# Performance work log

Hardware: AMD Instinct MI355X
Metric: run time of the kernel (lower is better)

The kernel has to match this reference:

```python
import jax, jax.numpy as jnp
import numpy as np


def setup_inputs() -> dict:
    key = jax.random.key(0)
    k1, k2, k3 = jax.random.split(key, 3)
    B, C, H, W = 4, 256, 96, 128
    F = 9
    return {
        "input1": jax.random.normal(k1, (B, C, H, W), dtype=jnp.float32),
        "input2": jax.random.normal(k2, (B, C, H, W), dtype=jnp.float32),
        "weights": jax.random.normal(k3, (C, F, F), dtype=jnp.float32),
        "filter_size": 9,
        "dilation": 2,
        "num_groups": 4,
    }


def _weighted_corr(input1, input2, weights, filter_size, dilation, num_groups):
    B, C, H, W = input1.shape
    F = filter_size
    G = num_groups
    Cg = C // G
    r = F // 2
    pad = r * dilation
    # zero-pad input2 spatially so out-of-bounds displacements contribute 0
    p2 = jnp.pad(input2, ((0, 0), (0, 0), (pad, pad), (pad, pad)))
    in1g = input1.reshape(B, G, Cg, H, W)
    outs = []  # one [B, G, H, W] map per window offset (dy, dx)
    for dy in range(F):
        for dx in range(F):
            shifted = p2[:, :, dy * dilation:dy * dilation + H,
                         dx * dilation:dx * dilation + W].reshape(B, G, Cg, H, W)
            wg = weights[:, dy, dx].reshape(G, Cg)
            outs.append(jnp.einsum('bgchw,bgchw,gc->bghw', in1g, shifted, wg))
    out = jnp.stack(outs, axis=2)  # [B, G, F*F, H, W]
    return out.reshape(B, G * F * F, H, W)


def reference(input1, input2, weights, filter_size, dilation, num_groups):
    return _weighted_corr(input1, input2, weights, filter_size, dilation, num_groups)
```

## Files before the change

kernel.cpp:

```cpp
#include <hip/hip_runtime.h>

#define B_   4
#define C_   256
#define H_   96
#define W_   128
#define F_   9
#define G_   4
#define CG   64
#define NC8  8
#define NO   81
#define HW_  (H_ * W_)

#define OROWS 4
#define TCOLS 144
#define PCOLS 72
#define NENT  (OROWS * 2 * PCOLS)
#define PNK   3

typedef _Float16 half2v __attribute__((ext_vector_type(2)));
typedef unsigned u32x4 __attribute__((ext_vector_type(4)));

__device__ __forceinline__ half2v u2h(unsigned u) {
    half2v h; __builtin_memcpy(&h, &u, 4); return h;
}
__device__ __forceinline__ unsigned h2u(half2v h) {
    unsigned u; __builtin_memcpy(&u, &h, 4); return u;
}
__device__ __forceinline__ half2v pkrtz(float a, float b) {
    auto r = __builtin_amdgcn_cvt_pkrtz(a, b);
    half2v h; __builtin_memcpy(&h, &r, 4); return h;
}
__device__ __forceinline__ unsigned pkrtz_u(float a, float b) {
    auto r = __builtin_amdgcn_cvt_pkrtz(a, b);
    unsigned u; __builtin_memcpy(&u, &r, 4); return u;
}

#if __has_builtin(__builtin_amdgcn_fdot2)
#define FDOT2(a, b, c) __builtin_amdgcn_fdot2((a), (b), (c), false)
#else
__device__ __forceinline__ float fdot2_fb(half2v a, half2v b, float c) {
    return c + (float)a[0] * (float)b[0] + (float)a[1] * (float)b[1];
}
#define FDOT2(a, b, c) fdot2_fb((a), (b), (c))
#endif

__device__ __forceinline__ int swz(int col2) {
    return col2 ^ ((col2 >> 3) & 7);
}

__global__ void pack_weights_kernel(const float* __restrict__ w,
                                    u32x4* __restrict__ wp) {
    int i = blockIdx.x * blockDim.x + threadIdx.x;
    if (i >= G_ * NC8 * NO) return;
    int o  = i % NO;
    int c8 = (i / NO) % NC8;
    int g  = i / (NO * NC8);
    const float* base = w + (size_t)(g * CG + 8 * c8) * NO + o;
    u32x4 r;
    r.x = pkrtz_u(base[0 * NO], base[1 * NO]);
    r.y = pkrtz_u(base[2 * NO], base[3 * NO]);
    r.z = pkrtz_u(base[4 * NO], base[5 * NO]);
    r.w = pkrtz_u(base[6 * NO], base[7 * NO]);
    wp[i] = r;
}

template <bool PACKED>
__global__ __launch_bounds__(256)
void wcorr_kernel(const float* __restrict__ in1, const float* __restrict__ in2,
                  const u32x4* __restrict__ wp, const float* __restrict__ wraw,
                  float* __restrict__ out) {
    __shared__ u32x4 tile[2][NENT];

    int bid   = blockIdx.x;
    int xcd   = bid & 7;
    int slot  = bid >> 3;
    int tuple = slot / 9;
    int dy    = slot - tuple * 9;
    int T     = tuple * 8 + xcd;
    int pair  = T & 15;
    int hblk  = T >> 4;
    int b = pair >> 2, g = pair & 3;
    int h0 = hblk * OROWS;

    int t   = threadIdx.x;
    int row = t >> 6;
    int i   = t & 63;
    int j   = i >> 1;
    int p   = i & 1;
    const int c0 = 4 * j + p;

    const float* in1g = in1 + (size_t)(b * C_ + g * CG) * HW_;
    const float* in2g = in2 + (size_t)(b * C_ + g * CG) * HW_;

    const int gr0 = h0 + 2 * dy - 8;
    int po[PNK]; unsigned msk[PNK]; int lix[PNK];
#pragma unroll
    for (int k = 0; k < PNK; ++k) {
        int pidx = k * 256 + t;
        int srow = pidx / TCOLS;
        int col  = pidx - srow * TCOLS;
        int gr = gr0 + srow, gc = col - 8;
        bool inb = (pidx < NENT) && gr >= 0 && gr < H_ && gc >= 0 && gc < W_;
        int off = gr * W_ + gc;
        off = off < 0 ? 0 : (off > HW_ - 1 ? HW_ - 1 : off);
        po[k]  = off;
        float m = inb ? 1.f : 0.f;
        msk[k] = pkrtz_u(m, m);
        lix[k] = (srow * 2 + (col & 1)) * PCOLS + swz(col >> 1);
    }

    int widx[10];
#pragma unroll
    for (int m = 0; m < 10; ++m)
        widx[m] = (row * 2 + p) * PCOLS + swz(2 * j + m);

    float acc0[F_], acc1[F_];
#pragma unroll
    for (int dx = 0; dx < F_; ++dx) { acc0[dx] = 0.f; acc1[dx] = 0.f; }

    float sv[PNK][8];

    auto LOADS = [&](int c8n) {
        const float* chb = in2g + (size_t)(8 * c8n) * HW_;
#pragma unroll
        for (int k = 0; k < PNK; ++k) {
            if (k < PNK - 1 || t < NENT - (PNK - 1) * 256) {
                const float* q = chb + po[k];
#pragma unroll
                for (int c = 0; c < 8; ++c) sv[k][c] = q[(size_t)c * HW_];
            }
        }
    };
    auto WRITE = [&](u32x4* dst) {
#pragma unroll
        for (int k = 0; k < PNK; ++k) {
            if (k < PNK - 1 || t < NENT - (PNK - 1) * 256) {
                half2v m = u2h(msk[k]);
                u32x4 e;
                e.x = h2u(u2h(pkrtz_u(sv[k][0], sv[k][1])) * m);
                e.y = h2u(u2h(pkrtz_u(sv[k][2], sv[k][3])) * m);
                e.z = h2u(u2h(pkrtz_u(sv[k][4], sv[k][5])) * m);
                e.w = h2u(u2h(pkrtz_u(sv[k][6], sv[k][7])) * m);
                dst[lix[k]] = e;
            }
        }
    };

    LOADS(0);
    WRITE(tile[0]);
    LOADS(1);

    const int in1off = (h0 + row) * W_ + c0;

    for (int c8 = 0; c8 < NC8; ++c8) {
        __syncthreads();

        if (c8 + 1 < NC8) WRITE(tile[(c8 + 1) & 1]);
        if (c8 + 2 < NC8) LOADS(c8 + 2);

        const float* ib = in1g + (size_t)(8 * c8) * HW_ + in1off;
        half2v ha0, ha1, ha2, ha3, hb0, hb1, hb2, hb3;
        {
            float x0 = ib[0], x1 = ib[HW_], x2 = ib[2 * HW_], x3 = ib[3 * HW_];
            float x4 = ib[4 * HW_], x5 = ib[5 * HW_], x6 = ib[6 * HW_], x7 = ib[7 * HW_];
            ha0 = pkrtz(x0, x1); ha1 = pkrtz(x2, x3);
            ha2 = pkrtz(x4, x5); ha3 = pkrtz(x6, x7);
            float y0 = ib[2], y1 = ib[HW_ + 2], y2 = ib[2 * HW_ + 2], y3 = ib[3 * HW_ + 2];
            float y4 = ib[4 * HW_ + 2], y5 = ib[5 * HW_ + 2], y6 = ib[6 * HW_ + 2], y7 = ib[7 * HW_ + 2];
            hb0 = pkrtz(y0, y1); hb1 = pkrtz(y2, y3);
            hb2 = pkrtz(y4, y5); hb3 = pkrtz(y6, y7);
        }

        const u32x4* lt = tile[c8 & 1];
        const u32x4* wrow = PACKED ? (wp + ((size_t)g * NC8 + c8) * NO + dy * F_) : nullptr;
        const float* wr = wraw + (size_t)(g * CG + 8 * c8) * NO + dy * F_;

#pragma unroll
        for (int m = 0; m < 10; ++m) {
            u32x4 uv = lt[widx[m]];
            if (m <= 8) {
                half2v w0h, w1h, w2h, w3h;
                if (PACKED) {
                    u32x4 wv = wrow[m];
                    w0h = u2h(wv.x); w1h = u2h(wv.y); w2h = u2h(wv.z); w3h = u2h(wv.w);
                } else {
                    w0h = pkrtz(wr[m + 0 * NO], wr[m + 1 * NO]);
                    w1h = pkrtz(wr[m + 2 * NO], wr[m + 3 * NO]);
                    w2h = pkrtz(wr[m + 4 * NO], wr[m + 5 * NO]);
                    w3h = pkrtz(wr[m + 6 * NO], wr[m + 7 * NO]);
                }
                float s = acc0[m];
                s = FDOT2(w0h * ha0, u2h(uv.x), s);
                s = FDOT2(w1h * ha1, u2h(uv.y), s);
                s = FDOT2(w2h * ha2, u2h(uv.z), s);
                s = FDOT2(w3h * ha3, u2h(uv.w), s);
                acc0[m] = s;
            }
            if (m >= 1) {
                const int dx = m - 1;
                half2v w0h, w1h, w2h, w3h;
                if (PACKED) {
                    u32x4 wv = wrow[dx];
                    w0h = u2h(wv.x); w1h = u2h(wv.y); w2h = u2h(wv.z); w3h = u2h(wv.w);
                } else {
                    w0h = pkrtz(wr[dx + 0 * NO], wr[dx + 1 * NO]);
                    w1h = pkrtz(wr[dx + 2 * NO], wr[dx + 3 * NO]);
                    w2h = pkrtz(wr[dx + 4 * NO], wr[dx + 5 * NO]);
                    w3h = pkrtz(wr[dx + 6 * NO], wr[dx + 7 * NO]);
                }
                float s = acc1[dx];
                s = FDOT2(w0h * hb0, u2h(uv.x), s);
                s = FDOT2(w1h * hb1, u2h(uv.y), s);
                s = FDOT2(w2h * hb2, u2h(uv.z), s);
                s = FDOT2(w3h * hb3, u2h(uv.w), s);
                acc1[dx] = s;
            }
        }
    }

    size_t obase = (((size_t)(pair * NO + dy * F_)) * H_ + (h0 + row)) * W_ + c0;
#pragma unroll
    for (int dx = 0; dx < F_; ++dx) {
        out[obase + (size_t)dx * HW_]     = acc0[dx];
        out[obase + (size_t)dx * HW_ + 2] = acc1[dx];
    }
}

extern "C" void kernel_launch(void* const* d_in, const int* in_sizes, int n_in,
                              void* d_out, int out_size, void* d_ws, size_t ws_size,
                              hipStream_t stream) {
    const float* in1  = (const float*)d_in[0];
    const float* in2  = (const float*)d_in[1];
    const float* wraw = (const float*)d_in[2];
    float* out = (float*)d_out;

    const size_t wp_bytes = (size_t)G_ * NC8 * NO * 16;
    const int nblocks = 8 * 48 * F_;

    if (ws_size >= wp_bytes) {
        u32x4* wp = (u32x4*)d_ws;
        int n = G_ * NC8 * NO;
        pack_weights_kernel<<<(n + 255) / 256, 256, 0, stream>>>(wraw, wp);
        wcorr_kernel<true><<<nblocks, 256, 0, stream>>>(in1, in2, wp, wraw, out);
    } else {
        wcorr_kernel<false><<<nblocks, 256, 0, stream>>>(in1, in2, nullptr, wraw, out);
    }
}
```

Before: 91.21 us.

## Replace XOR-swizzled LDS tile with padded stride and prefetch input1 one chunk ahead

Replaces the XOR swizzle on the shared-memory tile with a padded row stride of 73 entries, so LDS reads become a base pointer plus a constant offset and the per-thread index array goes away. Separately, the input1 values for the next channel chunk are now loaded one iteration early into registers, hiding global-load latency behind the dot-product loop. The costs are higher register pressure, slightly more LDS per block, and a possible change in bank-conflict behaviour for 16-byte accesses with the odd stride.

After: 90.09 us. About the same (-1.2%).

```diff
diff --git a/kernel.cpp b/kernel.cpp
--- a/kernel.cpp
+++ b/kernel.cpp
@@ -14,7 +14,9 @@
 #define OROWS 4
 #define TCOLS 144
 #define PCOLS 72
-#define NENT  (OROWS * 2 * PCOLS)
+#define PSTR  73
+#define NENT  (OROWS * 2 * PSTR)
+#define NPIX  (OROWS * TCOLS)
 #define PNK   3
 
 typedef _Float16 half2v __attribute__((ext_vector_type(2)));
@@ -43,10 +45,6 @@
 }
 #define FDOT2(a, b, c) fdot2_fb((a), (b), (c))
 #endif
-
-__device__ __forceinline__ int swz(int col2) {
-    return col2 ^ ((col2 >> 3) & 7);
-}
 
 __global__ void pack_weights_kernel(const float* __restrict__ w,
                                     u32x4* __restrict__ wp) {
@@ -100,19 +98,14 @@
         int srow = pidx / TCOLS;
         int col  = pidx - srow * TCOLS;
         int gr = gr0 + srow, gc = col - 8;
-        bool inb = (pidx < NENT) && gr >= 0 && gr < H_ && gc >= 0 && gc < W_;
+        bool inb = (pidx < NPIX) && gr >= 0 && gr < H_ && gc >= 0 && gc < W_;
         int off = gr * W_ + gc;
         off = off < 0 ? 0 : (off > HW_ - 1 ? HW_ - 1 : off);
         po[k]  = off;
         float m = inb ? 1.f : 0.f;
         msk[k] = pkrtz_u(m, m);
-        lix[k] = (srow * 2 + (col & 1)) * PCOLS + swz(col >> 1);
-    }
-
-    int widx[10];
-#pragma unroll
-    for (int m = 0; m < 10; ++m)
-        widx[m] = (row * 2 + p) * PCOLS + swz(2 * j + m);
+        lix[k] = (srow * 2 + (col & 1)) * PSTR + (col >> 1);
+    }
 
     float acc0[F_], acc1[F_];
 #pragma unroll
@@ -124,7 +117,7 @@
         const float* chb = in2g + (size_t)(8 * c8n) * HW_;
 #pragma unroll
         for (int k = 0; k < PNK; ++k) {
-            if (k < PNK - 1 || t < NENT - (PNK - 1) * 256) {
+            if (k < PNK - 1 || t < NPIX - (PNK - 1) * 256) {
                 const float* q = chb + po[k];
 #pragma unroll
                 for (int c = 0; c < 8; ++c) sv[k][c] = q[(size_t)c * HW_];
@@ -134,7 +127,7 @@
     auto WRITE = [&](u32x4* dst) {
 #pragma unroll
         for (int k = 0; k < PNK; ++k) {
-            if (k < PNK - 1 || t < NENT - (PNK - 1) * 256) {
+            if (k < PNK - 1 || t < NPIX - (PNK - 1) * 256) {
                 half2v m = u2h(msk[k]);
                 u32x4 e;
                 e.x = h2u(u2h(pkrtz_u(sv[k][0], sv[k][1])) * m);
@@ -151,6 +144,17 @@
     LOADS(1);
 
     const int in1off = (h0 + row) * W_ + c0;
+    float a[16];
+    {
+        const float* ib = in1g + in1off;
+#pragma unroll
+        for (int c = 0; c < 8; ++c) {
+            a[c]     = ib[(size_t)c * HW_];
+            a[8 + c] = ib[(size_t)c * HW_ + 2];
+        }
+    }
+
+    const int wb = (row * 2 + p) * PSTR + 2 * j;
 
     for (int c8 = 0; c8 < NC8; ++c8) {
         __syncthreads();
@@ -158,26 +162,26 @@
         if (c8 + 1 < NC8) WRITE(tile[(c8 + 1) & 1]);
         if (c8 + 2 < NC8) LOADS(c8 + 2);
 
-        const float* ib = in1g + (size_t)(8 * c8) * HW_ + in1off;
-        half2v ha0, ha1, ha2, ha3, hb0, hb1, hb2, hb3;
-        {
-            float x0 = ib[0], x1 = ib[HW_], x2 = ib[2 * HW_], x3 = ib[3 * HW_];
-            float x4 = ib[4 * HW_], x5 = ib[5 * HW_], x6 = ib[6 * HW_], x7 = ib[7 * HW_];
-            ha0 = pkrtz(x0, x1); ha1 = pkrtz(x2, x3);
-            ha2 = pkrtz(x4, x5); ha3 = pkrtz(x6, x7);
-            float y0 = ib[2], y1 = ib[HW_ + 2], y2 = ib[2 * HW_ + 2], y3 = ib[3 * HW_ + 2];
-            float y4 = ib[4 * HW_ + 2], y5 = ib[5 * HW_ + 2], y6 = ib[6 * HW_ + 2], y7 = ib[7 * HW_ + 2];
-            hb0 = pkrtz(y0, y1); hb1 = pkrtz(y2, y3);
-            hb2 = pkrtz(y4, y5); hb3 = pkrtz(y6, y7);
-        }
-
-        const u32x4* lt = tile[c8 & 1];
+        half2v ha0 = pkrtz(a[0], a[1]),  ha1 = pkrtz(a[2], a[3]);
+        half2v ha2 = pkrtz(a[4], a[5]),  ha3 = pkrtz(a[6], a[7]);
+        half2v hb0 = pkrtz(a[8], a[9]),  hb1 = pkrtz(a[10], a[11]);
+        half2v hb2 = pkrtz(a[12], a[13]), hb3 = pkrtz(a[14], a[15]);
+        if (c8 + 1 < NC8) {
+            const float* ib = in1g + (size_t)(8 * (c8 + 1)) * HW_ + in1off;
+#pragma unroll
+            for (int c = 0; c < 8; ++c) {
+                a[c]     = ib[(size_t)c * HW_];
+                a[8 + c] = ib[(size_t)c * HW_ + 2];
+            }
+        }
+
+        const u32x4* lt = tile[c8 & 1] + wb;
         const u32x4* wrow = PACKED ? (wp + ((size_t)g * NC8 + c8) * NO + dy * F_) : nullptr;
         const float* wr = wraw + (size_t)(g * CG + 8 * c8) * NO + dy * F_;
 
 #pragma unroll
         for (int m = 0; m < 10; ++m) {
-            u32x4 uv = lt[widx[m]];
+            u32x4 uv = lt[m];
             if (m <= 8) {
                 half2v w0h, w1h, w2h, w3h;
                 if (PACKED) {
```
